# Kernel optimization log

Measured on AMD Instinct MI355X. Metric: run time of the kernel, lower is better.

## Reference

```python
import jax, jax.numpy as jnp
import numpy as np

B, S, D_IN, D_H = 4, 2048, 1024, 1024

def setup_inputs() -> dict:
    key = jax.random.key(0)
    kx, kq, kk, kv = jax.random.split(key, 4)
    # nn.Linear default init: U(-1/sqrt(fan_in), 1/sqrt(fan_in)); stored as [out, in]
    bound = 1.0 / np.sqrt(D_IN)
    x = jax.random.normal(kx, (B, S, D_IN), dtype=jnp.float32)
    W_q = jax.random.uniform(kq, (D_H, D_IN), jnp.float32, -bound, bound)
    W_k = jax.random.uniform(kk, (D_H, D_IN), jnp.float32, -bound, bound)
    W_v = jax.random.uniform(kv, (D_H, D_IN), jnp.float32, -bound, bound)
    return {"x": x, "W_q": W_q, "W_k": W_k, "W_v": W_v}

def reference(x, W_q, W_k, W_v):
    # Q = x @ W_q.T, etc. (nn.Linear with bias=False)
    Q = jnp.einsum('bsd,hd->bsh', x, W_q)
    K = jnp.einsum('bsd,hd->bsh', x, W_k)
    V = jnp.einsum('bsd,hd->bsh', x, W_v)
    # NOTE: original scales by sqrt(Q.shape[1]) == sqrt(seq_len), not sqrt(d)
    scale = 1.0 / jnp.sqrt(jnp.asarray(Q.shape[1], Q.dtype))
    scores = jnp.einsum('bqh,bkh->bqk', Q, K) * scale  # [B,S,S]
    attn = jax.nn.softmax(scores, axis=-1)
    return jnp.einsum('bqk,bkh->bqh', attn, V)
```

## Files before the change

### kernel.cpp

```cpp
#include <hip/hip_runtime.h>

typedef unsigned short ushort_t;
typedef __attribute__((ext_vector_type(8))) __bf16 bf16x8;
typedef __attribute__((ext_vector_type(4))) float floatx4;

__device__ __forceinline__ ushort_t f2bf(float f) {
    unsigned int u = __builtin_bit_cast(unsigned int, f);
    u = (u + 0x7fffu + ((u >> 16) & 1u)) >> 16;
    return (ushort_t)u;
}

__device__ __forceinline__ void async16(const ushort_t* g, ushort_t* l) {
    __builtin_amdgcn_global_load_lds(
        (const __attribute__((address_space(1))) unsigned int*)g,
        (__attribute__((address_space(3))) unsigned int*)l,
        16 , 0 , 0 );
}

__device__ __forceinline__ int sw(int row, int cg) {
    return ((row << 2) + ((cg ^ row ^ (row >> 2)) & 3)) << 3;
}

__device__ __forceinline__ int xcd_swz(int bid, int cpx) {
    return (bid & 7) * cpx + (bid >> 3);
}

template <int N>
__device__ __forceinline__ void vwait() {
    if constexpr (N == 0)      asm volatile("s_waitcnt vmcnt(0)" ::: "memory");
    else if constexpr (N == 3) asm volatile("s_waitcnt vmcnt(3)" ::: "memory");
    else if constexpr (N == 4) asm volatile("s_waitcnt vmcnt(4)" ::: "memory");
    else if constexpr (N == 6) asm volatile("s_waitcnt vmcnt(6)" ::: "memory");
    else if constexpr (N == 8) asm volatile("s_waitcnt vmcnt(8)" ::: "memory");
    else static_assert(N == 0, "unsupported vmcnt");
}

template <int BM, int BN, int IM, int IN, int NW, int NS>
__device__ __forceinline__ void gemm_core_p(
    const ushort_t* __restrict__ A, int lda,
    const ushort_t* __restrict__ B, int ldb,
    int K, int tile_m, int tile_n,
    ushort_t* buf,
    floatx4 (&acc)[IM][IN]) {

    constexpr int NT = NW * 64;
    constexpr int SA = BM * 4 / NT;
    constexpr int SB = BN * 4 / NT;
    constexpr int Q  = SA + SB;
    constexpr int SLOT = (BM + BN) * 32;
    constexpr int BOFF = BM * 32;

    const int tid  = threadIdx.x;
    const int lane = tid & 63;
    const int wave = tid >> 6;
    const int wm   = wave >> 1, wn = wave & 1;
    const int quad = lane >> 4;
    const int l16  = lane & 15;

#pragma unroll
    for (int i = 0; i < IM; i++)
#pragma unroll
        for (int j = 0; j < IN; j++) acc[i][j] = (floatx4){0.f, 0.f, 0.f, 0.f};

    const ushort_t* ga[SA];
    int la[SA];
#pragma unroll
    for (int s = 0; s < SA; s++) {
        int seg = tid + s * NT;
        int r = seg >> 2, c = (seg ^ r ^ (r >> 2)) & 3;
        ga[s] = A + (long)(r + tile_m) * lda + c * 8;
        la[s] = seg * 8;
    }
    const ushort_t* gb[SB];
    int lb[SB];
#pragma unroll
    for (int s = 0; s < SB; s++) {
        int seg = tid + s * NT;
        int r = seg >> 2, c = (seg ^ r ^ (r >> 2)) & 3;
        gb[s] = B + (long)(r + tile_n) * ldb + c * 8;
        lb[s] = BOFF + seg * 8;
    }

    const int nk = K >> 5;

#pragma unroll
    for (int p = 0; p < NS - 1; ++p) {
#pragma unroll
        for (int s = 0; s < SA; s++) async16(ga[s] + p * 32, buf + p * SLOT + la[s]);
#pragma unroll
        for (int s = 0; s < SB; s++) async16(gb[s] + p * 32, buf + p * SLOT + lb[s]);
    }

    int slot = 0, slot2 = NS - 1;
    for (int k = 0; k < nk; ++k) {
        const int rem = nk - 1 - k;
        if (rem >= NS - 2) {
            vwait<(NS - 2) * Q>();
        } else if (NS >= 4 && rem == 1) {
            vwait<Q>();
        } else {
            vwait<0>();
        }
        __builtin_amdgcn_s_barrier();
        asm volatile("" ::: "memory");

        if (k + NS - 1 < nk) {
            const int koff = (k + NS - 1) << 5;
            ushort_t* dst = buf + slot2 * SLOT;
#pragma unroll
            for (int s = 0; s < SA; s++) async16(ga[s] + koff, dst + la[s]);
#pragma unroll
            for (int s = 0; s < SB; s++) async16(gb[s] + koff, dst + lb[s]);
        }

        const ushort_t* as = buf + slot * SLOT;
        const ushort_t* bs = as + BOFF;
        bf16x8 af[IM], bfr[IN];
#pragma unroll
        for (int im = 0; im < IM; im++)
            af[im] = *(const bf16x8*)&as[sw(wm * IM * 16 + im * 16 + l16, quad)];
#pragma unroll
        for (int in = 0; in < IN; in++)
            bfr[in] = *(const bf16x8*)&bs[sw(wn * IN * 16 + in * 16 + l16, quad)];
#pragma unroll
        for (int im = 0; im < IM; im++)
#pragma unroll
            for (int in = 0; in < IN; in++)
                acc[im][in] = __builtin_amdgcn_mfma_f32_16x16x32_bf16(
                    af[im], bfr[in], acc[im][in], 0, 0, 0);

        slot  = (slot == NS - 1) ? 0 : slot + 1;
        slot2 = (slot2 == NS - 1) ? 0 : slot2 + 1;
    }
}

__device__ __forceinline__ void gemm256_8ph(
    const ushort_t* __restrict__ A, int lda,
    const ushort_t* __restrict__ B, int ldb,
    int K, int tile_m, int tile_n,
    ushort_t* buf,
    floatx4 (&acc)[8][4]) {

    const int tid  = threadIdx.x;
    const int lane = tid & 63;
    const int wave = tid >> 6;
    const int wm   = wave >> 2;
    const int wn   = wave & 3;
    const int quad = lane >> 4;
    const int l16  = lane & 15;

#pragma unroll
    for (int i = 0; i < 8; i++)
#pragma unroll
        for (int j = 0; j < 4; j++) acc[i][j] = (floatx4){0.f, 0.f, 0.f, 0.f};

    const int srow = tid >> 3;
    const int scg  = (tid & 7) ^ (srow & 7);
    const ushort_t* gA = A + (long)(tile_m + srow) * lda + scg * 8;
    const ushort_t* gB = B + (long)(tile_n + srow) * ldb + scg * 8;
    ushort_t* const ld = buf + tid * 8;

#define STA_(p, h, t)                                                          \
    do {                                                                       \
        async16(gA + (long)((h)*128)      * lda + (t)*64,                      \
                ld + (p)*32768 + (h)*8192);                                    \
        async16(gA + (long)((h)*128 + 64) * lda + (t)*64,                      \
                ld + (p)*32768 + (h)*8192 + 4096);                             \
    } while (0)
#define STB_(p, h, t)                                                          \
    do {                                                                       \
        async16(gB + (long)((h)*128)      * ldb + (t)*64,                      \
                ld + (p)*32768 + 16384 + (h)*8192);                            \
        async16(gB + (long)((h)*128 + 64) * ldb + (t)*64,                      \
                ld + (p)*32768 + 16384 + (h)*8192 + 4096);                     \
    } while (0)

    const int rb0 = l16 * 64 + (((quad)     ^ (l16 & 7)) << 3);
    const int rb1 = l16 * 64 + (((quad + 4) ^ (l16 & 7)) << 3);
    const int abase = wm * 8192;
    const int bbase = 16384 + (wn >> 1) * 8192 + (wn & 1) * 4096;

    const int nt = K >> 6;

    STA_(0, 0, 0); STB_(0, 0, 0); STB_(0, 1, 0); STA_(0, 1, 0);
    STB_(1, 0, 1); STB_(1, 1, 1); STA_(1, 0, 1);
    asm volatile("s_waitcnt vmcnt(6)" ::: "memory");
    __builtin_amdgcn_s_barrier();
    asm volatile("" ::: "memory");

    bf16x8 aR[4][2], bKc[2][2], bCc[2][2];

    for (int t = 0; t < nt; ++t) {
        const int p  = t & 1;
        const int pn = p ^ 1;
        const ushort_t* sb = buf + p * 32768;

        if (t + 1 < nt) STA_(pn, 1, t + 1);
#pragma unroll
        for (int fr = 0; fr < 4; fr++) {
            aR[fr][0] = *(const bf16x8*)&sb[abase + fr * 1024 + rb0];
            aR[fr][1] = *(const bf16x8*)&sb[abase + fr * 1024 + rb1];
        }
#pragma unroll
        for (int fc = 0; fc < 2; fc++) {
            bKc[fc][0] = *(const bf16x8*)&sb[bbase + fc * 1024 + rb0];
            bKc[fc][1] = *(const bf16x8*)&sb[bbase + fc * 1024 + rb1];
        }
        asm volatile("" ::: "memory");
        __builtin_amdgcn_s_barrier();
        __builtin_amdgcn_s_setprio(1);
#pragma unroll
        for (int fr = 0; fr < 4; fr++)
#pragma unroll
            for (int fc = 0; fc < 2; fc++) {
                acc[fr][fc] = __builtin_amdgcn_mfma_f32_16x16x32_bf16(
                    aR[fr][0], bKc[fc][0], acc[fr][fc], 0, 0, 0);
                acc[fr][fc] = __builtin_amdgcn_mfma_f32_16x16x32_bf16(
                    aR[fr][1], bKc[fc][1], acc[fr][fc], 0, 0, 0);
            }
        __builtin_amdgcn_s_setprio(0);
        asm volatile("" ::: "memory");
        __builtin_amdgcn_s_barrier();
        asm volatile("" ::: "memory");

#pragma unroll
        for (int fc = 0; fc < 2; fc++) {
            bCc[fc][0] = *(const bf16x8*)&sb[bbase + (fc + 2) * 1024 + rb0];
            bCc[fc][1] = *(const bf16x8*)&sb[bbase + (fc + 2) * 1024 + rb1];
        }
        asm volatile("" ::: "memory");
        __builtin_amdgcn_s_barrier();
        __builtin_amdgcn_s_setprio(1);
#pragma unroll
        for (int fr = 0; fr < 4; fr++)
#pragma unroll
            for (int fc = 0; fc < 2; fc++) {
                acc[fr][fc + 2] = __builtin_amdgcn_mfma_f32_16x16x32_bf16(
                    aR[fr][0], bCc[fc][0], acc[fr][fc + 2], 0, 0, 0);
                acc[fr][fc + 2] = __builtin_amdgcn_mfma_f32_16x16x32_bf16(
                    aR[fr][1], bCc[fc][1], acc[fr][fc + 2], 0, 0, 0);
            }
        __builtin_amdgcn_s_setprio(0);
        asm volatile("" ::: "memory");
        __builtin_amdgcn_s_barrier();
        asm volatile("" ::: "memory");

        if (t + 2 < nt) STB_(p, 0, t + 2);
#pragma unroll
        for (int fr = 0; fr < 4; fr++) {
            aR[fr][0] = *(const bf16x8*)&sb[abase + (fr + 4) * 1024 + rb0];
            aR[fr][1] = *(const bf16x8*)&sb[abase + (fr + 4) * 1024 + rb1];
        }
        asm volatile("" ::: "memory");
        __builtin_amdgcn_s_barrier();
        __builtin_amdgcn_s_setprio(1);
#pragma unroll
        for (int fr = 0; fr < 4; fr++)
#pragma unroll
            for (int fc = 0; fc < 2; fc++) {
                acc[fr + 4][fc + 2] = __builtin_amdgcn_mfma_f32_16x16x32_bf16(
                    aR[fr][0], bCc[fc][0], acc[fr + 4][fc + 2], 0, 0, 0);
                acc[fr + 4][fc + 2] = __builtin_amdgcn_mfma_f32_16x16x32_bf16(
                    aR[fr][1], bCc[fc][1], acc[fr + 4][fc + 2], 0, 0, 0);
            }
        __builtin_amdgcn_s_setprio(0);
        asm volatile("" ::: "memory");
        __builtin_amdgcn_s_barrier();
        asm volatile("" ::: "memory");

        if (t + 2 < nt) { STB_(p, 1, t + 2); STA_(p, 0, t + 2); }
        asm volatile("" ::: "memory");
        __builtin_amdgcn_s_barrier();
        __builtin_amdgcn_s_setprio(1);
#pragma unroll
        for (int fr = 0; fr < 4; fr++)
#pragma unroll
            for (int fc = 0; fc < 2; fc++) {
                acc[fr + 4][fc] = __builtin_amdgcn_mfma_f32_16x16x32_bf16(
                    aR[fr][0], bKc[fc][0], acc[fr + 4][fc], 0, 0, 0);
                acc[fr + 4][fc] = __builtin_amdgcn_mfma_f32_16x16x32_bf16(
                    aR[fr][1], bKc[fc][1], acc[fr + 4][fc], 0, 0, 0);
            }
        __builtin_amdgcn_s_setprio(0);
        if (t + 2 < nt) vwait<6>();
        else            vwait<0>();
        __builtin_amdgcn_s_barrier();
        asm volatile("" ::: "memory");
    }
#undef STA_
#undef STB_
}

__global__ void prep_kernel(const float* __restrict__ x,
                            const float* __restrict__ wq,
                            const float* __restrict__ wk,
                            const float* __restrict__ wv,
                            ushort_t* __restrict__ xb,
                            ushort_t* __restrict__ wvb,
                            ushort_t* __restrict__ wqT,
                            ushort_t* __restrict__ wkT,
                            float* __restrict__ lsum) {
    const int bx = blockIdx.x;
    const int t = threadIdx.x;
    if (bx < 9216) {
        const float* src;
        ushort_t* dst;
        long g;
        if (bx < 8192) { src = x;  dst = xb;  g = ((long)bx * 256 + t) * 4; }
        else           { src = wv; dst = wvb; g = ((long)(bx - 8192) * 256 + t) * 4; }
        float4 v = *(const float4*)(src + g);
        ushort4 o;
        o.x = f2bf(v.x); o.y = f2bf(v.y); o.z = f2bf(v.z); o.w = f2bf(v.w);
        *(ushort4*)(dst + g) = o;
        return;
    }
    if (bx < 9224) {
        int idx = (bx - 9216) * 256 + t;
        ((float4*)lsum)[idx] = (float4){0.f, 0.f, 0.f, 0.f};
        return;
    }
    const int tt = bx - 9224;
    const float* src = (tt >= 256) ? wk : wq;
    ushort_t* dst = (tt >= 256) ? wkT : wqT;
    const int id = tt & 255;
    const int h0 = (id >> 4) * 64, d0 = (id & 15) * 64;
    __shared__ ushort_t tile[64 * 80];
    {
        int i = t >> 2, cg = (t & 3) << 4;
        const float4* p = (const float4*)(src + (long)(h0 + i) * 1024 + d0 + cg);
#pragma unroll
        for (int k = 0; k < 4; k++) {
            float4 v = p[k];
            ushort_t* q = &tile[i * 80 + cg + k * 4];
            q[0] = f2bf(v.x); q[1] = f2bf(v.y); q[2] = f2bf(v.z); q[3] = f2bf(v.w);
        }
    }
    __syncthreads();
    {
        int j = t >> 2, ig = (t & 3) << 4;
        ushort_t tmp[16];
#pragma unroll
        for (int k = 0; k < 16; k++) tmp[k] = tile[(ig + k) * 80 + j];
        ushort_t* o = dst + (long)(d0 + j) * 1024 + h0 + ig;
        *(uint4*)o = ((uint4*)tmp)[0];
        *(uint4*)(o + 8) = ((uint4*)tmp)[1];
    }
}

__global__ __launch_bounds__(512, 4) void gv_kernel(
    const ushort_t* __restrict__ wkT, const ushort_t* __restrict__ wqT,
    const ushort_t* __restrict__ wvb, const ushort_t* __restrict__ xb,
    ushort_t* __restrict__ Gb, ushort_t* __restrict__ VTb) {

    __shared__ __align__(16) ushort_t buf[3 * 384 * 32];

    const ushort_t *A, *B;
    ushort_t* C;
    int ldc, tile_m, tile_n;
    if (blockIdx.x < 32) {
        A = wkT; B = wqT; C = Gb; ldc = 1024;
        tile_m = (blockIdx.x >> 3) * 256;
        tile_n = (blockIdx.x & 7) * 128;
    } else {
        int id = blockIdx.x - 32;
        A = wvb; B = xb; C = VTb; ldc = 8192;
        tile_m = (id >> 6) * 256;
        tile_n = (id & 63) * 128;
    }

    floatx4 acc[4][4];
    gemm_core_p<256, 128, 4, 4, 8, 3>(A, 1024, B, 1024, 1024, tile_m, tile_n, buf, acc);

    const int lane = threadIdx.x & 63, wave = threadIdx.x >> 6;
    const int wm = wave >> 1, wn = wave & 1, quad = lane >> 4, l16 = lane & 15;
#pragma unroll
    for (int im = 0; im < 4; im++)
#pragma unroll
        for (int r = 0; r < 4; r++) {
            int row = tile_m + wm * 64 + im * 16 + quad * 4 + r;
#pragma unroll
            for (int in = 0; in < 4; in++) {
                int col = tile_n + wn * 64 + in * 16 + l16;
                C[(long)row * ldc + col] = f2bf(acc[im][in][r]);
            }
        }
}

__global__ __launch_bounds__(256) void y_kernel(
    const ushort_t* __restrict__ xb,
    const ushort_t* __restrict__ Gb,
    ushort_t* __restrict__ Yb) {

    __shared__ __align__(16) ushort_t buf[4 * 256 * 32];
    const int lin = xcd_swz(blockIdx.x, 64);
    const int tile_n = (lin & 7) * 128;
    const int tile_m = (lin >> 3) * 128;

    floatx4 acc[4][4];
    gemm_core_p<128, 128, 4, 4, 4, 4>(xb, 1024, Gb, 1024, 1024, tile_m, tile_n, buf, acc);

    const int lane = threadIdx.x & 63, wave = threadIdx.x >> 6;
    const int wm = wave >> 1, wn = wave & 1, quad = lane >> 4, l16 = lane & 15;
#pragma unroll
    for (int im = 0; im < 4; im++)
#pragma unroll
        for (int r = 0; r < 4; r++) {
            int row = tile_m + wm * 64 + im * 16 + quad * 4 + r;
#pragma unroll
            for (int in = 0; in < 4; in++) {
                int col = tile_n + wn * 64 + in * 16 + l16;
                Yb[(long)row * 1024 + col] = f2bf(acc[im][in][r]);
            }
        }
}

__global__ __launch_bounds__(512, 2) void pexp_kernel(
    const ushort_t* __restrict__ Yb,
    const ushort_t* __restrict__ xb,
    ushort_t* __restrict__ Pb,
    float* __restrict__ lsum) {

    __shared__ __align__(16) ushort_t buf[65536];

    const int lin = xcd_swz(blockIdx.x, 32);
    const int z = lin >> 6;
    const int tile_m = ((lin >> 3) & 7) * 256;
    const int tile_n = (lin & 7) * 256;

    const ushort_t* A = Yb + (long)z * 2097152;
    const ushort_t* B = xb + (long)z * 2097152;
    ushort_t* C = Pb + (long)z * 4194304;
    float* l = lsum + z * 2048;

    floatx4 acc[8][4];
    gemm256_8ph(A, 1024, B, 1024, 1024, tile_m, tile_n, buf, acc);

    const float scale = 0.022097086912079608f;
    const int lane = threadIdx.x & 63, wave = threadIdx.x >> 6;
    const int wm = wave >> 2, wn = wave & 3, quad = lane >> 4, l16 = lane & 15;
#pragma unroll
    for (int fr = 0; fr < 8; fr++)
#pragma unroll
        for (int rr = 0; rr < 4; rr++) {
            int row = tile_m + wm * 128 + fr * 16 + quad * 4 + rr;
            float psum = 0.f;
#pragma unroll
            for (int fc = 0; fc < 4; fc++) {
                int col = tile_n + wn * 64 + fc * 16 + l16;
                float e = __expf(acc[fr][fc][rr] * scale);
                C[(long)row * 2048 + col] = f2bf(e);
                psum += e;
            }
            psum += __shfl_xor(psum, 1, 64);
            psum += __shfl_xor(psum, 2, 64);
            psum += __shfl_xor(psum, 4, 64);
            psum += __shfl_xor(psum, 8, 64);
            if (l16 == 0) atomicAdd(&l[row], psum);
        }
}

__global__ __launch_bounds__(256) void out_kernel(
    const ushort_t* __restrict__ Pb,
    const ushort_t* __restrict__ VTb,
    float* __restrict__ out,
    const float* __restrict__ lsum) {

    __shared__ __align__(16) ushort_t buf[4 * 256 * 32];

    const int lin = xcd_swz(blockIdx.x, 64);
    const int z = lin >> 7;
    const int tile_m = ((lin >> 3) & 15) * 128;
    const int tile_n = (lin & 7) * 128;

    const ushort_t* A = Pb + (long)z * 4194304;
    const ushort_t* B = VTb + (long)z * 2048;
    float* C = out + (long)z * 2097152;
    const float* l = lsum + z * 2048;

    floatx4 acc[4][4];
    gemm_core_p<128, 128, 4, 4, 4, 4>(A, 2048, B, 8192, 2048, tile_m, tile_n, buf, acc);

    const int lane = threadIdx.x & 63, wave = threadIdx.x >> 6;
    const int wm = wave >> 1, wn = wave & 1, quad = lane >> 4, l16 = lane & 15;
#pragma unroll
    for (int im = 0; im < 4; im++)
#pragma unroll
        for (int r = 0; r < 4; r++) {
            int row = tile_m + wm * 64 + im * 16 + quad * 4 + r;
            float li = 1.0f / l[row];
#pragma unroll
            for (int in = 0; in < 4; in++) {
                int col = tile_n + wn * 64 + in * 16 + l16;
                C[(long)row * 1024 + col] = acc[im][in][r] * li;
            }
        }
}

extern "C" void kernel_launch(void* const* d_in, const int* in_sizes, int n_in,
                              void* d_out, int out_size, void* d_ws, size_t ws_size,
                              hipStream_t stream) {
    const float* x  = (const float*)d_in[0];
    const float* wq = (const float*)d_in[1];
    const float* wk = (const float*)d_in[2];
    const float* wv = (const float*)d_in[3];

    ushort_t* xb  = (ushort_t*)d_ws;
    ushort_t* wvb = xb  + 8388608;
    ushort_t* wqT = wvb + 1048576;
    ushort_t* wkT = wqT + 1048576;
    ushort_t* Gb  = wkT + 1048576;
    ushort_t* Yb  = Gb  + 1048576;
    ushort_t* VTb = Yb  + 8388608;
    ushort_t* Pb  = VTb + 8388608;
    float*    lsum = (float*)(Pb + 16777216);
    float*    out  = (float*)d_out;

    prep_kernel<<<9736, 256, 0, stream>>>(x, wq, wk, wv, xb, wvb, wqT, wkT, lsum);
    gv_kernel<<<288, 512, 0, stream>>>(wkT, wqT, wvb, xb, Gb, VTb);
    y_kernel<<<512, 256, 0, stream>>>(xb, Gb, Yb);
    pexp_kernel<<<256, 512, 0, stream>>>(Yb, xb, Pb, lsum);
    out_kernel<<<512, 256, 0, stream>>>(Pb, VTb, out, lsum);
}
```

Baseline: 230.9 us.

## Use 128x256 two-phase GEMM tiles with 8 waves for y and out kernels

Adds a new GEMM core with 128x256 block tiles, 512 threads and two MFMA phases per k-step, and switches y_kernel and out_kernel to it with half as many blocks. The aim is more reuse of each A tile and fewer blocks, which cuts global and LDS traffic per FLOP. It also swaps compiler memory clobbers for sched_barrier plus explicit lgkmcnt waits and moves async stores after the LDS reads in the existing pipelined core, so loads can overlap better. The cost is higher register and LDS pressure, and fewer blocks may leave CUs underfilled at 256 blocks.

```diff
diff --git a/kernel.cpp b/kernel.cpp
--- a/kernel.cpp
+++ b/kernel.cpp
@@ -34,6 +34,8 @@
     else if constexpr (N == 8) asm volatile("s_waitcnt vmcnt(8)" ::: "memory");
     else static_assert(N == 0, "unsupported vmcnt");
 }
+
+#define SBAR0() __builtin_amdgcn_sched_barrier(0)
 
 template <int BM, int BN, int IM, int IN, int NW, int NS>
 __device__ __forceinline__ void gemm_core_p(
@@ -184,9 +186,10 @@
 
     STA_(0, 0, 0); STB_(0, 0, 0); STB_(0, 1, 0); STA_(0, 1, 0);
     STB_(1, 0, 1); STB_(1, 1, 1); STA_(1, 0, 1);
-    asm volatile("s_waitcnt vmcnt(6)" ::: "memory");
+    asm volatile("s_waitcnt vmcnt(6)");
+    SBAR0();
     __builtin_amdgcn_s_barrier();
-    asm volatile("" ::: "memory");
+    SBAR0();
 
     bf16x8 aR[4][2], bKc[2][2], bCc[2][2];
 
@@ -195,7 +198,6 @@
         const int pn = p ^ 1;
         const ushort_t* sb = buf + p * 32768;
 
-        if (t + 1 < nt) STA_(pn, 1, t + 1);
 #pragma unroll
         for (int fr = 0; fr < 4; fr++) {
             aR[fr][0] = *(const bf16x8*)&sb[abase + fr * 1024 + rb0];
@@ -206,8 +208,12 @@
             bKc[fc][0] = *(const bf16x8*)&sb[bbase + fc * 1024 + rb0];
             bKc[fc][1] = *(const bf16x8*)&sb[bbase + fc * 1024 + rb1];
         }
-        asm volatile("" ::: "memory");
-        __builtin_amdgcn_s_barrier();
+        if (t + 1 < nt) STA_(pn, 1, t + 1);
+        asm volatile("s_waitcnt lgkmcnt(8)");
+        SBAR0();
+        __builtin_amdgcn_s_barrier();
+        asm volatile("s_waitcnt lgkmcnt(0)");
+        SBAR0();
         __builtin_amdgcn_s_setprio(1);
 #pragma unroll
         for (int fr = 0; fr < 4; fr++)
@@ -219,17 +225,19 @@
                     aR[fr][1], bKc[fc][1], acc[fr][fc], 0, 0, 0);
             }
         __builtin_amdgcn_s_setprio(0);
-        asm volatile("" ::: "memory");
-        __builtin_amdgcn_s_barrier();
-        asm volatile("" ::: "memory");
+        SBAR0();
+        __builtin_amdgcn_s_barrier();
+        SBAR0();
 
 #pragma unroll
         for (int fc = 0; fc < 2; fc++) {
             bCc[fc][0] = *(const bf16x8*)&sb[bbase + (fc + 2) * 1024 + rb0];
             bCc[fc][1] = *(const bf16x8*)&sb[bbase + (fc + 2) * 1024 + rb1];
         }
-        asm volatile("" ::: "memory");
-        __builtin_amdgcn_s_barrier();
+        SBAR0();
+        __builtin_amdgcn_s_barrier();
+        asm volatile("s_waitcnt lgkmcnt(0)");
+        SBAR0();
         __builtin_amdgcn_s_setprio(1);
 #pragma unroll
         for (int fr = 0; fr < 4; fr++)
@@ -241,18 +249,20 @@
                     aR[fr][1], bCc[fc][1], acc[fr][fc + 2], 0, 0, 0);
             }
         __builtin_amdgcn_s_setprio(0);
-        asm volatile("" ::: "memory");
-        __builtin_amdgcn_s_barrier();
-        asm volatile("" ::: "memory");
-
-        if (t + 2 < nt) STB_(p, 0, t + 2);
+        SBAR0();
+        __builtin_amdgcn_s_barrier();
+        SBAR0();
+
 #pragma unroll
         for (int fr = 0; fr < 4; fr++) {
             aR[fr][0] = *(const bf16x8*)&sb[abase + (fr + 4) * 1024 + rb0];
             aR[fr][1] = *(const bf16x8*)&sb[abase + (fr + 4) * 1024 + rb1];
         }
-        asm volatile("" ::: "memory");
-        __builtin_amdgcn_s_barrier();
+        if (t + 2 < nt) STB_(p, 0, t + 2);
+        SBAR0();
+        __builtin_amdgcn_s_barrier();
+        asm volatile("s_waitcnt lgkmcnt(0)");
+        SBAR0();
         __builtin_amdgcn_s_setprio(1);
 #pragma unroll
         for (int fr = 0; fr < 4; fr++)
@@ -264,13 +274,14 @@
                     aR[fr][1], bCc[fc][1], acc[fr + 4][fc + 2], 0, 0, 0);
             }
         __builtin_amdgcn_s_setprio(0);
-        asm volatile("" ::: "memory");
-        __builtin_amdgcn_s_barrier();
-        asm volatile("" ::: "memory");
+        SBAR0();
+        __builtin_amdgcn_s_barrier();
+        SBAR0();
 
         if (t + 2 < nt) { STB_(p, 1, t + 2); STA_(p, 0, t + 2); }
-        asm volatile("" ::: "memory");
-        __builtin_amdgcn_s_barrier();
+        SBAR0();
+        __builtin_amdgcn_s_barrier();
+        SBAR0();
         __builtin_amdgcn_s_setprio(1);
 #pragma unroll
         for (int fr = 0; fr < 4; fr++)
@@ -282,13 +293,143 @@
                     aR[fr][1], bKc[fc][1], acc[fr + 4][fc], 0, 0, 0);
             }
         __builtin_amdgcn_s_setprio(0);
-        if (t + 2 < nt) vwait<6>();
-        else            vwait<0>();
-        __builtin_amdgcn_s_barrier();
-        asm volatile("" ::: "memory");
+        if (t + 2 < nt) asm volatile("s_waitcnt vmcnt(6)");
+        else            asm volatile("s_waitcnt vmcnt(0)");
+        SBAR0();
+        __builtin_amdgcn_s_barrier();
+        SBAR0();
     }
 #undef STA_
 #undef STB_
+}
+
+__device__ __forceinline__ void gemm_bn256_2ph(
+    const ushort_t* __restrict__ A, int lda,
+    const ushort_t* __restrict__ B, int ldb,
+    int K, int tile_m, int tile_n,
+    ushort_t* buf,
+    floatx4 (&acc)[4][4]) {
+
+    const int tid  = threadIdx.x;
+    const int lane = tid & 63;
+    const int wave = tid >> 6;
+    const int wm   = wave >> 2;
+    const int wn   = wave & 3;
+    const int quad = lane >> 4;
+    const int l16  = lane & 15;
+
+#pragma unroll
+    for (int i = 0; i < 4; i++)
+#pragma unroll
+        for (int j = 0; j < 4; j++) acc[i][j] = (floatx4){0.f, 0.f, 0.f, 0.f};
+
+    const int srow = tid >> 3;
+    const int scg  = (tid & 7) ^ (srow & 7);
+    const ushort_t* gA = A + (long)(tile_m + srow) * lda + scg * 8;
+    const ushort_t* gB = B + (long)(tile_n + srow) * ldb + scg * 8;
+    ushort_t* const ld = buf + tid * 8;
+
+#define SAU_(p, t)                                                             \
+    do {                                                                       \
+        async16(gA + (long)(t)*64,            ld + (p)*24576);                 \
+        async16(gA + (long)64*lda  + (t)*64,  ld + (p)*24576 + 4096);          \
+    } while (0)
+#define SB0_(p, t)                                                             \
+    do {                                                                       \
+        async16(gB + (long)(t)*64,            ld + (p)*24576 + 8192);          \
+        async16(gB + (long)64*ldb  + (t)*64,  ld + (p)*24576 + 12288);         \
+    } while (0)
+#define SB1_(p, t)                                                             \
+    do {                                                                       \
+        async16(gB + (long)128*ldb + (t)*64,  ld + (p)*24576 + 16384);         \
+        async16(gB + (long)192*ldb + (t)*64,  ld + (p)*24576 + 20480);         \
+    } while (0)
+
+    const int rb0 = l16 * 64 + (((quad)     ^ (l16 & 7)) << 3);
+    const int rb1 = l16 * 64 + (((quad + 4) ^ (l16 & 7)) << 3);
+    const int ab = wm * 4096;
+    const int bb = 8192 + wn * 1024;
+
+    const int nt = K >> 6;
+
+    SAU_(0, 0); SB0_(0, 0); SB1_(0, 0);
+    SAU_(1, 1); SB0_(1, 1);
+    asm volatile("s_waitcnt vmcnt(4)");
+    SBAR0();
+    __builtin_amdgcn_s_barrier();
+    SBAR0();
+
+    bf16x8 aR[4][2], bKc[2][2], bCc[2][2];
+
+    for (int t = 0; t < nt; ++t) {
+        const int p  = t & 1;
+        const int pn = p ^ 1;
+        const ushort_t* sb = buf + p * 24576;
+
+#pragma unroll
+        for (int fr = 0; fr < 4; fr++) {
+            aR[fr][0] = *(const bf16x8*)&sb[ab + fr * 1024 + rb0];
+            aR[fr][1] = *(const bf16x8*)&sb[ab + fr * 1024 + rb1];
+        }
+#pragma unroll
+        for (int fc = 0; fc < 2; fc++) {
+            bKc[fc][0] = *(const bf16x8*)&sb[bb + fc * 4096 + rb0];
+            bKc[fc][1] = *(const bf16x8*)&sb[bb + fc * 4096 + rb1];
+        }
+        if (t + 1 < nt) SB1_(pn, t + 1);
+        asm volatile("s_waitcnt lgkmcnt(8)");
+        SBAR0();
+        __builtin_amdgcn_s_barrier();
+        asm volatile("s_waitcnt lgkmcnt(0)");
+        SBAR0();
+        __builtin_amdgcn_s_setprio(1);
+#pragma unroll
+        for (int fr = 0; fr < 4; fr++)
+#pragma unroll
+            for (int fc = 0; fc < 2; fc++) {
+                acc[fr][fc] = __builtin_amdgcn_mfma_f32_16x16x32_bf16(
+                    aR[fr][0], bKc[fc][0], acc[fr][fc], 0, 0, 0);
+                acc[fr][fc] = __builtin_amdgcn_mfma_f32_16x16x32_bf16(
+                    aR[fr][1], bKc[fc][1], acc[fr][fc], 0, 0, 0);
+            }
+        __builtin_amdgcn_s_setprio(0);
+        if (t + 1 < nt) asm volatile("s_waitcnt vmcnt(6)");
+        else            asm volatile("s_waitcnt vmcnt(0)");
+        SBAR0();
+        __builtin_amdgcn_s_barrier();
+        SBAR0();
+
+#pragma unroll
+        for (int fc = 0; fc < 2; fc++) {
+            bCc[fc][0] = *(const bf16x8*)&sb[bb + (fc + 2) * 4096 + rb0];
+            bCc[fc][1] = *(const bf16x8*)&sb[bb + (fc + 2) * 4096 + rb1];
+        }
+        if (t + 2 < nt) { SAU_(p, t + 2); SB0_(p, t + 2); }
+        SBAR0();
+        __builtin_amdgcn_s_barrier();
+        asm volatile("s_waitcnt lgkmcnt(0)");
+        SBAR0();
+        __builtin_amdgcn_s_setprio(1);
+#pragma unroll
+        for (int fr = 0; fr < 4; fr++)
+#pragma unroll
+            for (int fc = 0; fc < 2; fc++) {
+                acc[fr][fc + 2] = __builtin_amdgcn_mfma_f32_16x16x32_bf16(
+                    aR[fr][0], bCc[fc][0], acc[fr][fc + 2], 0, 0, 0);
+                acc[fr][fc + 2] = __builtin_amdgcn_mfma_f32_16x16x32_bf16(
+                    aR[fr][1], bCc[fc][1], acc[fr][fc + 2], 0, 0, 0);
+            }
+        __builtin_amdgcn_s_setprio(0);
+        if (t + 2 < nt)      asm volatile("s_waitcnt vmcnt(6)");
+        else if (t + 1 < nt) asm volatile("s_waitcnt vmcnt(2)");
+        else                 asm volatile("s_waitcnt vmcnt(0)");
+        SBAR0();
+        __builtin_amdgcn_s_barrier();
+        SBAR0();
+    }
+#undef SAU_
+#undef SB0_
+#undef SB1_
 }
 
 __global__ void prep_kernel(const float* __restrict__ x,
@@ -386,30 +527,30 @@
         }
 }
 
-__global__ __launch_bounds__(256) void y_kernel(
+__global__ __launch_bounds__(512, 2) void y_kernel(
     const ushort_t* __restrict__ xb,
     const ushort_t* __restrict__ Gb,
     ushort_t* __restrict__ Yb) {
 
-    __shared__ __align__(16) ushort_t buf[4 * 256 * 32];
-    const int lin = xcd_swz(blockIdx.x, 64);
-    const int tile_n = (lin & 7) * 128;
-    const int tile_m = (lin >> 3) * 128;
+    __shared__ __align__(16) ushort_t buf[49152];
+    const int lin = xcd_swz(blockIdx.x, 32);
+    const int tile_m = (lin >> 2) * 128;
+    const int tile_n = (lin & 3) * 256;
 
     floatx4 acc[4][4];
-    gemm_core_p<128, 128, 4, 4, 4, 4>(xb, 1024, Gb, 1024, 1024, tile_m, tile_n, buf, acc);
+    gemm_bn256_2ph(xb, 1024, Gb, 1024, 1024, tile_m, tile_n, buf, acc);
 
     const int lane = threadIdx.x & 63, wave = threadIdx.x >> 6;
-    const int wm = wave >> 1, wn = wave & 1, quad = lane >> 4, l16 = lane & 15;
-#pragma unroll
-    for (int im = 0; im < 4; im++)
+    const int wm = wave >> 2, wn = wave & 3, quad = lane >> 4, l16 = lane & 15;
+#pragma unroll
+    for (int fr = 0; fr < 4; fr++)
 #pragma unroll
         for (int r = 0; r < 4; r++) {
-            int row = tile_m + wm * 64 + im * 16 + quad * 4 + r;
-#pragma unroll
-            for (int in = 0; in < 4; in++) {
-                int col = tile_n + wn * 64 + in * 16 + l16;
-                Yb[(long)row * 1024 + col] = f2bf(acc[im][in][r]);
+            int row = tile_m + wm * 64 + fr * 16 + quad * 4 + r;
+#pragma unroll
+            for (int fc = 0; fc < 4; fc++) {
+                int col = tile_n + fc * 64 + wn * 16 + l16;
+                Yb[(long)row * 1024 + col] = f2bf(acc[fr][fc][r]);
             }
         }
 }
@@ -459,18 +600,18 @@
         }
 }
 
-__global__ __launch_bounds__(256) void out_kernel(
+__global__ __launch_bounds__(512, 2) void out_kernel(
     const ushort_t* __restrict__ Pb,
     const ushort_t* __restrict__ VTb,
     float* __restrict__ out,
     const float* __restrict__ lsum) {
 
-    __shared__ __align__(16) ushort_t buf[4 * 256 * 32];
-
-    const int lin = xcd_swz(blockIdx.x, 64);
-    const int z = lin >> 7;
-    const int tile_m = ((lin >> 3) & 15) * 128;
-    const int tile_n = (lin & 7) * 128;
+    __shared__ __align__(16) ushort_t buf[49152];
+
+    const int lin = xcd_swz(blockIdx.x, 32);
+    const int z = lin >> 6;
+    const int tile_m = ((lin >> 2) & 15) * 128;
+    const int tile_n = (lin & 3) * 256;
 
     const ushort_t* A = Pb + (long)z * 4194304;
     const ushort_t* B = VTb + (long)z * 2048;
@@ -478,20 +619,20 @@
     const float* l = lsum + z * 2048;
 
     floatx4 acc[4][4];
-    gemm_core_p<128, 128, 4, 4, 4, 4>(A, 2048, B, 8192, 2048, tile_m, tile_n, buf, acc);
+    gemm_bn256_2ph(A, 2048, B, 8192, 2048, tile_m, tile_n, buf, acc);
 
     const int lane = threadIdx.x & 63, wave = threadIdx.x >> 6;
-    const int wm = wave >> 1, wn = wave & 1, quad = lane >> 4, l16 = lane & 15;
-#pragma unroll
-    for (int im = 0; im < 4; im++)
+    const int wm = wave >> 2, wn = wave & 3, quad = lane >> 4, l16 = lane & 15;
+#pragma unroll
+    for (int fr = 0; fr < 4; fr++)
 #pragma unroll
         for (int r = 0; r < 4; r++) {
-            int row = tile_m + wm * 64 + im * 16 + quad * 4 + r;
+            int row = tile_m + wm * 64 + fr * 16 + quad * 4 + r;
             float li = 1.0f / l[row];
 #pragma unroll
-            for (int in = 0; in < 4; in++) {
-                int col = tile_n + wn * 64 + in * 16 + l16;
-                C[(long)row * 1024 + col] = acc[im][in][r] * li;
+            for (int fc = 0; fc < 4; fc++) {
+                int col = tile_n + fc * 64 + wn * 16 + l16;
+                C[(long)row * 1024 + col] = acc[fr][fc][r] * li;
             }
         }
 }
@@ -517,7 +658,7 @@
 
     prep_kernel<<<9736, 256, 0, stream>>>(x, wq, wk, wv, xb, wvb, wqT, wkT, lsum);
     gv_kernel<<<288, 512, 0, stream>>>(wkT, wqT, wvb, xb, Gb, VTb);
-    y_kernel<<<512, 256, 0, stream>>>(xb, Gb, Yb);
+    y_kernel<<<256, 512, 0, stream>>>(xb, Gb, Yb);
     pexp_kernel<<<256, 512, 0, stream>>>(Yb, xb, Pb, lsum);
-    out_kernel<<<512, 256, 0, stream>>>(Pb, VTb, out, lsum);
-}
+    out_kernel<<<256, 512, 0, stream>>>(Pb, VTb, out, lsum);
+}
```

Result: no change. 230.4 us (-0.2%).
